# Performance work log

Hardware: AMD Instinct MI355X
Metric: run time of the kernel (lower is better)

## Reference

```python
import jax, jax.numpy as jnp
import numpy as np

B, T, D = 64, 4096, 256
UNITS = 256  # must equal D due to the module's build() wiring


def setup_inputs() -> dict:
    key = jax.random.key(0)
    k1, k2, k3 = jax.random.split(key, 3)
    inputs = jax.random.normal(k1, (B, T, D), dtype=jnp.float32)
    # Glorot-uniform-ish init for Dense kernels, zeros for biases (Keras defaults)
    lim_w = np.sqrt(6.0 / (D + UNITS)).astype(np.float32)
    W_w = jax.random.uniform(k2, (D, UNITS), jnp.float32, -lim_w, lim_w)
    W_b = jnp.zeros((UNITS,), jnp.float32)
    lim_v = np.sqrt(6.0 / (UNITS + 1)).astype(np.float32)
    V_w = jax.random.uniform(k3, (UNITS, 1), jnp.float32, -lim_v, lim_v)
    V_b = jnp.zeros((1,), jnp.float32)
    return {"inputs": inputs, "W_w": W_w, "W_b": W_b, "V_w": V_w, "V_b": V_b}


def reference(inputs, W_w, W_b, V_w, V_b):
    # score: [B, T, UNITS]
    score = jnp.tanh(jnp.einsum('btd,du->btu', inputs, W_w) + W_b)
    # logits: [B, T, 1]; softmax over time axis (axis=1)
    logits = jnp.einsum('btu,uo->bto', score, V_w) + V_b
    attn = jax.nn.softmax(logits, axis=1)  # [B, T, 1]
    # weighted sum over time -> [B, D]
    context = jnp.sum(attn * inputs, axis=1)
    return context
```

## Files before the change

kernel.cpp:

```cpp
#include <hip/hip_runtime.h>
#include <hip/hip_bf16.h>
#include <math.h>

#define BB 64
#define TT 4096
#define DD 256
#define UU 256
#define MT 32
#define NT (TT/MT)
#define LDA 264

typedef __attribute__((ext_vector_type(8))) short bf16x8;
typedef __attribute__((ext_vector_type(4))) float f32x4;

static __device__ __forceinline__ short f2bf(float f){
  unsigned u = __float_as_uint(f);
  u = (u + 0x7fffu + ((u >> 16) & 1u)) >> 16;
  return (short)u;
}

static __device__ __forceinline__ unsigned pk_bf16(float a, float b){
#if __has_builtin(__builtin_amdgcn_cvt_pk_bf16_f32)
  typedef __bf16 bf16v2 __attribute__((ext_vector_type(2)));
  bf16v2 r = __builtin_amdgcn_cvt_pk_bf16_f32(a, b);
  unsigned u; __builtin_memcpy(&u, &r, 4); return u;
#else
  unsigned ua = __float_as_uint(a), ub = __float_as_uint(b);
  ua = (ua + 0x7fffu + ((ua >> 16) & 1u)) >> 16;
  ub = (ub + 0x7fffu + ((ub >> 16) & 1u)) & 0xffff0000u;
  return ub | ua;
#endif
}

__global__ void wfrag_kernel(const float* __restrict__ W, short* __restrict__ Wf){
  int g  = blockIdx.x*256 + threadIdx.x;
  int l  = g & 63;
  int f  = g >> 6;
  int kt = f & 7, nf = (f >> 3) & 3, wv = f >> 5;
  int lo = l & 15, quad = l >> 4;
  int u  = wv*64 + nf*16 + lo;
  int d0 = kt*32 + quad*8;
  bf16x8 v;
  #pragma unroll
  for (int j=0;j<8;++j) v[j] = f2bf(W[(size_t)(d0+j)*UU + u]);
  *reinterpret_cast<bf16x8*>(&Wf[(size_t)g*8]) = v;
}

__global__ __launch_bounds__(256, 5)
void attn_tile_kernel(const float* __restrict__ X, const short* __restrict__ Wf,
                      const float* __restrict__ Wb, const float* __restrict__ Vw,
                      float* __restrict__ m_part, float* __restrict__ l_part,
                      float* __restrict__ ctx_part)
{
  __shared__ short a_tile[MT*LDA];
  __shared__ float s_part[4][MT];
  __shared__ float s_pw[4][MT];
  __shared__ float s_red[8][264];

  const int tid  = threadIdx.x;
  const int lane = tid & 63;
  const int wv   = tid >> 6;
  const int lo   = lane & 15;
  const int quad = lane >> 4;
  const int u_base = wv*64 + lo;
  const int b  = blockIdx.x >> 7;
  const int tt = blockIdx.x & 127;
  const size_t xbase = ((size_t)b*TT + (size_t)tt*MT)*DD;
  const int rgrp  = tid >> 5;
  const int cbase = (tid & 31)*8;

  float wb_r[4], v_r[4];
  #pragma unroll
  for (int nf=0; nf<4; ++nf){
    wb_r[nf] = Wb[u_base + nf*16];
    v_r[nf]  = Vw[u_base + nf*16];
  }
  const short* wf_base = Wf + ((size_t)(wv*32*64 + lane))*8;

  #pragma unroll
  for (int p8=0; p8<4; ++p8){
    const float4* src = reinterpret_cast<const float4*>(
        X + xbase + (size_t)(p8*8 + rgrp)*DD + cbase);
    float4 x0 = src[0];
    float4 x1 = src[1];
    int4 v;
    v.x = (int)pk_bf16(x0.x, x0.y);
    v.y = (int)pk_bf16(x0.z, x0.w);
    v.z = (int)pk_bf16(x1.x, x1.y);
    v.w = (int)pk_bf16(x1.z, x1.w);
    *reinterpret_cast<int4*>(&a_tile[(p8*8 + rgrp)*LDA + cbase]) = v;
  }
  __syncthreads();

  f32x4 acc[2][4];
  #pragma unroll
  for (int mf=0; mf<2; ++mf)
    #pragma unroll
    for (int nf=0; nf<4; ++nf)
      acc[mf][nf] = (f32x4){0.f,0.f,0.f,0.f};

  #pragma unroll
  for (int kt=0; kt<8; ++kt){
    const int k0 = kt*32 + quad*8;
    bf16x8 af[2];
    #pragma unroll
    for (int mf=0; mf<2; ++mf)
      af[mf] = *reinterpret_cast<const bf16x8*>(&a_tile[(mf*16 + lo)*LDA + k0]);
    #pragma unroll
    for (int nf=0; nf<4; ++nf){
      bf16x8 bfv = *reinterpret_cast<const bf16x8*>(wf_base + (nf*8 + kt)*512);
      #pragma unroll
      for (int mf=0; mf<2; ++mf)
        acc[mf][nf] = __builtin_amdgcn_mfma_f32_16x16x32_bf16(af[mf], bfv, acc[mf][nf], 0, 0, 0);
    }
  }

  #pragma unroll
  for (int mf=0; mf<2; ++mf){
    #pragma unroll
    for (int r=0; r<4; ++r){
      float part = 0.f;
      #pragma unroll
      for (int nf=0; nf<4; ++nf){
        float s  = acc[mf][nf][r] + wb_r[nf];
        float e2 = __expf(2.f*s);
        float th = 1.f - 2.f/(e2 + 1.f);
        part = fmaf(th, v_r[nf], part);
      }
      part += __shfl_xor(part, 1);
      part += __shfl_xor(part, 2);
      part += __shfl_xor(part, 4);
      part += __shfl_xor(part, 8);
      if (lo == 0) s_part[wv][mf*16 + quad*4 + r] = part;
    }
  }
  __syncthreads();

  const int li = lane & 31;
  float lt = s_part[0][li] + s_part[1][li] + s_part[2][li] + s_part[3][li];
  float mx = lt;
  #pragma unroll
  for (int o=16; o; o>>=1) mx = fmaxf(mx, __shfl_xor(mx, o));
  float p = __expf(lt - mx);
  float sum = p;
  #pragma unroll
  for (int o=16; o; o>>=1) sum += __shfl_xor(sum, o);
  s_pw[wv][li] = p;

  float cp[8] = {0.f,0.f,0.f,0.f,0.f,0.f,0.f,0.f};
  #pragma unroll
  for (int p8=0; p8<4; ++p8){
    float pr = s_pw[wv][p8*8 + rgrp];
    bf16x8 xv = *reinterpret_cast<const bf16x8*>(&a_tile[(p8*8 + rgrp)*LDA + cbase]);
    #pragma unroll
    for (int j=0; j<8; ++j){
      float x = __uint_as_float(((unsigned)(unsigned short)xv[j]) << 16);
      cp[j] = fmaf(pr, x, cp[j]);
    }
  }
  *reinterpret_cast<float4*>(&s_red[rgrp][cbase])   = (float4){cp[0],cp[1],cp[2],cp[3]};
  *reinterpret_cast<float4*>(&s_red[rgrp][cbase+4]) = (float4){cp[4],cp[5],cp[6],cp[7]};
  __syncthreads();

  float ctx = 0.f;
  #pragma unroll
  for (int g=0; g<8; ++g) ctx += s_red[g][tid];

  if (tid == 0){ m_part[blockIdx.x] = mx; l_part[blockIdx.x] = sum; }
  ctx_part[(size_t)blockIdx.x*DD + tid] = ctx;
}

__global__ __launch_bounds__(1024)
void merge_kernel(const float* __restrict__ m_part, const float* __restrict__ l_part,
                  const float* __restrict__ ctx_part, float* __restrict__ out)
{
  __shared__ float s_sum[4][256];
  const int b = blockIdx.x;
  const int g = threadIdx.x >> 8;
  const int d = threadIdx.x & 255;

  float mg = -INFINITY;
  #pragma unroll 16
  for (int i=0; i<NT; ++i) mg = fmaxf(mg, m_part[b*NT+i]);
  float lg = 0.f;
  #pragma unroll 16
  for (int i=0; i<NT; ++i) lg += l_part[b*NT+i] * __expf(m_part[b*NT+i] - mg);

  float s = 0.f;
  #pragma unroll 8
  for (int i=0; i<32; ++i){
    int t = g*32 + i;
    float w = __expf(m_part[b*NT+t] - mg);
    s = fmaf(w, ctx_part[(size_t)(b*NT+t)*DD + d], s);
  }
  s_sum[g][d] = s;
  __syncthreads();
  if (threadIdx.x < 256){
    float tot = s_sum[0][threadIdx.x] + s_sum[1][threadIdx.x]
              + s_sum[2][threadIdx.x] + s_sum[3][threadIdx.x];
    out[b*DD + threadIdx.x] = tot / lg;
  }
}

extern "C" void kernel_launch(void* const* d_in, const int* in_sizes, int n_in,
                              void* d_out, int out_size, void* d_ws, size_t ws_size,
                              hipStream_t stream)
{
  const float* X  = (const float*)d_in[0];
  const float* Ww = (const float*)d_in[1];
  const float* Wb = (const float*)d_in[2];
  const float* Vw = (const float*)d_in[3];
  float* out = (float*)d_out;

  short* Wf       = (short*)d_ws;
  float* m_part   = (float*)((char*)d_ws + (size_t)UU*DD*sizeof(short));
  float* l_part   = m_part + BB*NT;
  float* ctx_part = l_part + BB*NT;

  wfrag_kernel<<<32, 256, 0, stream>>>(Ww, Wf);
  attn_tile_kernel<<<BB*NT, 256, 0, stream>>>(X, Wf, Wb, Vw, m_part, l_part, ctx_part);
  merge_kernel<<<BB, 1024, 0, stream>>>(m_part, l_part, ctx_part, out);
}
```

Measured before the change: 419.3 us.

## Make tile blocks persistent over 8 time tiles with online softmax and prefetch

Each block now processes 8 consecutive 32-row time tiles instead of one. It keeps the W fragments resident in registers, prefetches the next tile's X into registers while computing the current one, and merges tiles with a running max/sum (online softmax). This removes the per-tile W reloads, partial writes and launch overhead. It also shrinks the merge kernel to 16 partials per batch. The cost is heavy register pressure (launch bounds lowered to 2) and double-buffered LDS, which reduce occupancy and latency hiding.

```diff
diff --git a/kernel.cpp b/kernel.cpp
--- a/kernel.cpp
+++ b/kernel.cpp
@@ -8,6 +8,9 @@
 #define UU 256
 #define MT 32
 #define NT (TT/MT)
+#define TPB 8
+#define NBLK (BB*NT/TPB)
+#define NP (NT/TPB)
 #define LDA 264
 
 typedef __attribute__((ext_vector_type(8))) short bf16x8;
@@ -46,13 +49,13 @@
   *reinterpret_cast<bf16x8*>(&Wf[(size_t)g*8]) = v;
 }
 
-__global__ __launch_bounds__(256, 5)
+__global__ __launch_bounds__(256, 2)
 void attn_tile_kernel(const float* __restrict__ X, const short* __restrict__ Wf,
                       const float* __restrict__ Wb, const float* __restrict__ Vw,
                       float* __restrict__ m_part, float* __restrict__ l_part,
                       float* __restrict__ ctx_part)
 {
-  __shared__ short a_tile[MT*LDA];
+  __shared__ short a_tile[2][MT*LDA];
   __shared__ float s_part[4][MT];
   __shared__ float s_pw[4][MT];
   __shared__ float s_red[8][264];
@@ -63,9 +66,10 @@
   const int lo   = lane & 15;
   const int quad = lane >> 4;
   const int u_base = wv*64 + lo;
-  const int b  = blockIdx.x >> 7;
-  const int tt = blockIdx.x & 127;
-  const size_t xbase = ((size_t)b*TT + (size_t)tt*MT)*DD;
+  const int blk = blockIdx.x;
+  const int b   = blk >> 4;
+  const int seg = blk & 15;
+  const size_t xbase0 = ((size_t)b*TT + (size_t)(seg*TPB)*MT)*DD;
   const int rgrp  = tid >> 5;
   const int cbase = (tid & 31)*8;
 
@@ -75,89 +79,130 @@
     wb_r[nf] = Wb[u_base + nf*16];
     v_r[nf]  = Vw[u_base + nf*16];
   }
-  const short* wf_base = Wf + ((size_t)(wv*32*64 + lane))*8;
-
+
+  bf16x8 wreg[4][8];
+  {
+    const short* wf_base = Wf + ((size_t)(wv*32*64 + lane))*8;
+    #pragma unroll
+    for (int nf=0; nf<4; ++nf)
+      #pragma unroll
+      for (int kt=0; kt<8; ++kt)
+        wreg[nf][kt] = *reinterpret_cast<const bf16x8*>(wf_base + (nf*8 + kt)*512);
+  }
+
+  float4 xp[8];
   #pragma unroll
   for (int p8=0; p8<4; ++p8){
     const float4* src = reinterpret_cast<const float4*>(
-        X + xbase + (size_t)(p8*8 + rgrp)*DD + cbase);
-    float4 x0 = src[0];
-    float4 x1 = src[1];
-    int4 v;
-    v.x = (int)pk_bf16(x0.x, x0.y);
-    v.y = (int)pk_bf16(x0.z, x0.w);
-    v.z = (int)pk_bf16(x1.x, x1.y);
-    v.w = (int)pk_bf16(x1.z, x1.w);
-    *reinterpret_cast<int4*>(&a_tile[(p8*8 + rgrp)*LDA + cbase]) = v;
-  }
-  __syncthreads();
-
-  f32x4 acc[2][4];
-  #pragma unroll
-  for (int mf=0; mf<2; ++mf)
-    #pragma unroll
-    for (int nf=0; nf<4; ++nf)
-      acc[mf][nf] = (f32x4){0.f,0.f,0.f,0.f};
-
-  #pragma unroll
-  for (int kt=0; kt<8; ++kt){
-    const int k0 = kt*32 + quad*8;
-    bf16x8 af[2];
+        X + xbase0 + (size_t)(p8*8 + rgrp)*DD + cbase);
+    xp[p8*2]   = src[0];
+    xp[p8*2+1] = src[1];
+  }
+
+  float m_run = -INFINITY, l_run = 0.f;
+  float cp[8] = {0.f,0.f,0.f,0.f,0.f,0.f,0.f,0.f};
+
+  for (int it=0; it<TPB; ++it){
+    const int buf = it & 1;
+
+    #pragma unroll
+    for (int p8=0; p8<4; ++p8){
+      int4 v;
+      v.x = (int)pk_bf16(xp[p8*2].x,   xp[p8*2].y);
+      v.y = (int)pk_bf16(xp[p8*2].z,   xp[p8*2].w);
+      v.z = (int)pk_bf16(xp[p8*2+1].x, xp[p8*2+1].y);
+      v.w = (int)pk_bf16(xp[p8*2+1].z, xp[p8*2+1].w);
+      *reinterpret_cast<int4*>(&a_tile[buf][(p8*8 + rgrp)*LDA + cbase]) = v;
+    }
+    __syncthreads();
+
+    if (it+1 < TPB){
+      const size_t xb = xbase0 + (size_t)(it+1)*MT*DD;
+      #pragma unroll
+      for (int p8=0; p8<4; ++p8){
+        const float4* src = reinterpret_cast<const float4*>(
+            X + xb + (size_t)(p8*8 + rgrp)*DD + cbase);
+        xp[p8*2]   = src[0];
+        xp[p8*2+1] = src[1];
+      }
+    }
+
+    f32x4 acc[2][4];
     #pragma unroll
     for (int mf=0; mf<2; ++mf)
-      af[mf] = *reinterpret_cast<const bf16x8*>(&a_tile[(mf*16 + lo)*LDA + k0]);
-    #pragma unroll
-    for (int nf=0; nf<4; ++nf){
-      bf16x8 bfv = *reinterpret_cast<const bf16x8*>(wf_base + (nf*8 + kt)*512);
+      #pragma unroll
+      for (int nf=0; nf<4; ++nf)
+        acc[mf][nf] = (f32x4){0.f,0.f,0.f,0.f};
+
+    #pragma unroll
+    for (int kt=0; kt<8; ++kt){
+      const int k0 = kt*32 + quad*8;
+      bf16x8 af[2];
       #pragma unroll
       for (int mf=0; mf<2; ++mf)
-        acc[mf][nf] = __builtin_amdgcn_mfma_f32_16x16x32_bf16(af[mf], bfv, acc[mf][nf], 0, 0, 0);
-    }
-  }
-
-  #pragma unroll
-  for (int mf=0; mf<2; ++mf){
-    #pragma unroll
-    for (int r=0; r<4; ++r){
-      float part = 0.f;
+        af[mf] = *reinterpret_cast<const bf16x8*>(&a_tile[buf][(mf*16 + lo)*LDA + k0]);
       #pragma unroll
       for (int nf=0; nf<4; ++nf){
-        float s  = acc[mf][nf][r] + wb_r[nf];
-        float e2 = __expf(2.f*s);
-        float th = 1.f - 2.f/(e2 + 1.f);
-        part = fmaf(th, v_r[nf], part);
-      }
-      part += __shfl_xor(part, 1);
-      part += __shfl_xor(part, 2);
-      part += __shfl_xor(part, 4);
-      part += __shfl_xor(part, 8);
-      if (lo == 0) s_part[wv][mf*16 + quad*4 + r] = part;
-    }
-  }
-  __syncthreads();
-
-  const int li = lane & 31;
-  float lt = s_part[0][li] + s_part[1][li] + s_part[2][li] + s_part[3][li];
-  float mx = lt;
-  #pragma unroll
-  for (int o=16; o; o>>=1) mx = fmaxf(mx, __shfl_xor(mx, o));
-  float p = __expf(lt - mx);
-  float sum = p;
-  #pragma unroll
-  for (int o=16; o; o>>=1) sum += __shfl_xor(sum, o);
-  s_pw[wv][li] = p;
-
-  float cp[8] = {0.f,0.f,0.f,0.f,0.f,0.f,0.f,0.f};
-  #pragma unroll
-  for (int p8=0; p8<4; ++p8){
-    float pr = s_pw[wv][p8*8 + rgrp];
-    bf16x8 xv = *reinterpret_cast<const bf16x8*>(&a_tile[(p8*8 + rgrp)*LDA + cbase]);
-    #pragma unroll
-    for (int j=0; j<8; ++j){
-      float x = __uint_as_float(((unsigned)(unsigned short)xv[j]) << 16);
-      cp[j] = fmaf(pr, x, cp[j]);
-    }
-  }
+        #pragma unroll
+        for (int mf=0; mf<2; ++mf)
+          acc[mf][nf] = __builtin_amdgcn_mfma_f32_16x16x32_bf16(af[mf], wreg[nf][kt], acc[mf][nf], 0, 0, 0);
+      }
+    }
+
+    #pragma unroll
+    for (int mf=0; mf<2; ++mf){
+      #pragma unroll
+      for (int r=0; r<4; ++r){
+        float part = 0.f;
+        #pragma unroll
+        for (int nf=0; nf<4; ++nf){
+          float s  = acc[mf][nf][r] + wb_r[nf];
+          float e2 = __expf(2.f*s);
+          float th = 1.f - 2.f/(e2 + 1.f);
+          part = fmaf(th, v_r[nf], part);
+        }
+        part += __shfl_xor(part, 1);
+        part += __shfl_xor(part, 2);
+        part += __shfl_xor(part, 4);
+        part += __shfl_xor(part, 8);
+        if (lo == 0) s_part[wv][mf*16 + quad*4 + r] = part;
+      }
+    }
+    __syncthreads();
+
+    const int li = lane & 31;
+    float lt = s_part[0][li] + s_part[1][li] + s_part[2][li] + s_part[3][li];
+    float mx = lt;
+    #pragma unroll
+    for (int o=16; o; o>>=1) mx = fmaxf(mx, __shfl_xor(mx, o));
+
+    float m_new = fmaxf(m_run, mx);
+    float corr  = __expf(m_run - m_new);
+    float p = __expf(lt - m_new);
+    float sum = p;
+    #pragma unroll
+    for (int o=16; o; o>>=1) sum += __shfl_xor(sum, o);
+    l_run = l_run * corr + sum;
+    s_pw[wv][li] = p;
+
+    if (corr != 1.f){
+      #pragma unroll
+      for (int j=0; j<8; ++j) cp[j] *= corr;
+    }
+    m_run = m_new;
+
+    #pragma unroll
+    for (int p8=0; p8<4; ++p8){
+      float pr = s_pw[wv][p8*8 + rgrp];
+      bf16x8 xv = *reinterpret_cast<const bf16x8*>(&a_tile[buf][(p8*8 + rgrp)*LDA + cbase]);
+      #pragma unroll
+      for (int j=0; j<8; ++j){
+        float x = __uint_as_float(((unsigned)(unsigned short)xv[j]) << 16);
+        cp[j] = fmaf(pr, x, cp[j]);
+      }
+    }
+  }
+
   *reinterpret_cast<float4*>(&s_red[rgrp][cbase])   = (float4){cp[0],cp[1],cp[2],cp[3]};
   *reinterpret_cast<float4*>(&s_red[rgrp][cbase+4]) = (float4){cp[4],cp[5],cp[6],cp[7]};
   __syncthreads();
@@ -166,40 +211,29 @@
   #pragma unroll
   for (int g=0; g<8; ++g) ctx += s_red[g][tid];
 
-  if (tid == 0){ m_part[blockIdx.x] = mx; l_part[blockIdx.x] = sum; }
-  ctx_part[(size_t)blockIdx.x*DD + tid] = ctx;
-}
-
-__global__ __launch_bounds__(1024)
+  if (tid == 0){ m_part[blk] = m_run; l_part[blk] = l_run; }
+  ctx_part[(size_t)blk*DD + tid] = ctx;
+}
+
+__global__ __launch_bounds__(256)
 void merge_kernel(const float* __restrict__ m_part, const float* __restrict__ l_part,
                   const float* __restrict__ ctx_part, float* __restrict__ out)
 {
-  __shared__ float s_sum[4][256];
   const int b = blockIdx.x;
-  const int g = threadIdx.x >> 8;
-  const int d = threadIdx.x & 255;
+  const int d = threadIdx.x;
 
   float mg = -INFINITY;
-  #pragma unroll 16
-  for (int i=0; i<NT; ++i) mg = fmaxf(mg, m_part[b*NT+i]);
-  float lg = 0.f;
-  #pragma unroll 16
-  for (int i=0; i<NT; ++i) lg += l_part[b*NT+i] * __expf(m_part[b*NT+i] - mg);
-
-  float s = 0.f;
-  #pragma unroll 8
-  for (int i=0; i<32; ++i){
-    int t = g*32 + i;
-    float w = __expf(m_part[b*NT+t] - mg);
-    s = fmaf(w, ctx_part[(size_t)(b*NT+t)*DD + d], s);
-  }
-  s_sum[g][d] = s;
-  __syncthreads();
-  if (threadIdx.x < 256){
-    float tot = s_sum[0][threadIdx.x] + s_sum[1][threadIdx.x]
-              + s_sum[2][threadIdx.x] + s_sum[3][threadIdx.x];
-    out[b*DD + threadIdx.x] = tot / lg;
-  }
+  #pragma unroll
+  for (int i=0; i<NP; ++i) mg = fmaxf(mg, m_part[b*NP+i]);
+
+  float lg = 0.f, s = 0.f;
+  #pragma unroll
+  for (int i=0; i<NP; ++i){
+    float w = __expf(m_part[b*NP+i] - mg);
+    lg += l_part[b*NP+i] * w;
+    s   = fmaf(w, ctx_part[(size_t)(b*NP+i)*DD + d], s);
+  }
+  out[b*DD + d] = s / lg;
 }
 
 extern "C" void kernel_launch(void* const* d_in, const int* in_sizes, int n_in,
@@ -214,10 +248,10 @@
 
   short* Wf       = (short*)d_ws;
   float* m_part   = (float*)((char*)d_ws + (size_t)UU*DD*sizeof(short));
-  float* l_part   = m_part + BB*NT;
-  float* ctx_part = l_part + BB*NT;
+  float* l_part   = m_part + NBLK;
+  float* ctx_part = l_part + NBLK;
 
   wfrag_kernel<<<32, 256, 0, stream>>>(Ww, Wf);
-  attn_tile_kernel<<<BB*NT, 256, 0, stream>>>(X, Wf, Wb, Vw, m_part, l_part, ctx_part);
-  merge_kernel<<<BB, 1024, 0, stream>>>(m_part, l_part, ctx_part, out);
-}
+  attn_tile_kernel<<<NBLK, 256, 0, stream>>>(X, Wf, Wb, Vw, m_part, l_part, ctx_part);
+  merge_kernel<<<BB, 256, 0, stream>>>(m_part, l_part, ctx_part, out);
+}
```

After: 382.1 us. 8.9% less time.
